# Performance work log

Hardware: AMD Instinct MI355X
Metric: run time of the kernel (lower is better)

## Reference

```python
import jax, jax.numpy as jnp
import numpy as np

C = 256
CK = C // 8  # qk projection dim


def setup_inputs() -> dict:
    key = jax.random.key(0)
    ks = jax.random.split(key, 8)
    B, H, W = 4, 64, 64
    x = jax.random.normal(ks[0], (B, C, W, H), dtype=jnp.float32)
    s = 1.0 / np.sqrt(C)
    Wf = jax.random.normal(ks[1], (CK, C), dtype=jnp.float32) * s
    bf = jax.random.normal(ks[2], (CK,), dtype=jnp.float32) * 0.01
    Wg = jax.random.normal(ks[3], (CK, C), dtype=jnp.float32) * s
    bg = jax.random.normal(ks[4], (CK,), dtype=jnp.float32) * 0.01
    Wh = jax.random.normal(ks[5], (C, C), dtype=jnp.float32) * s
    bh = jax.random.normal(ks[6], (C,), dtype=jnp.float32) * 0.01
    gamma = jax.random.normal(ks[7], (1,), dtype=jnp.float32) * 0.1
    return {"x": x, "Wf": Wf, "bf": bf, "Wg": Wg, "bg": bg,
            "Wh": Wh, "bh": bh, "gamma": gamma}


def reference(x, Wf, bf, Wg, bg, Wh, bh, gamma):
    B, Cc, Wd, Hd = x.shape
    N = Wd * Hd
    xf = x.reshape(B, Cc, N)  # B C N
    # 1x1 conv1d == channel matmul
    f = jnp.einsum('oc,bcn->bon', Wf, xf) + bf[None, :, None]  # B CK N
    g = jnp.einsum('oc,bcn->bon', Wg, xf) + bg[None, :, None]  # B CK N
    h = jnp.einsum('oc,bcn->bon', Wh, xf) + bh[None, :, None]  # B C N
    # s[b,i,j] = sum_k f[b,k,i] g[b,k,j]
    s = jnp.einsum('bki,bkj->bij', f, g)  # B N N
    attention = jax.nn.softmax(s, axis=-1)
    # out[b,c,i] = sum_j h[b,c,j] attention[b,i,j]
    out = jnp.einsum('bcj,bij->bci', h, attention)  # B C N
    out = out.reshape(B, Cc, Wd, Hd)
    return gamma[0] * out + x
```

## Files before the change

kernel.cpp:

```cpp
#include <hip/hip_runtime.h>

typedef __bf16 bf16x8 __attribute__((ext_vector_type(8)));
typedef __bf16 bf16x4 __attribute__((ext_vector_type(4)));
typedef float f32x4 __attribute__((ext_vector_type(4)));
typedef float f32x16 __attribute__((ext_vector_type(16)));

__device__ __forceinline__ f32x4 mfma16(bf16x8 a, bf16x8 b, f32x4 c) {
  return __builtin_amdgcn_mfma_f32_16x16x32_bf16(a, b, c, 0, 0, 0);
}
__device__ __forceinline__ f32x16 mfma32(bf16x8 a, bf16x8 b, f32x16 c) {
  return __builtin_amdgcn_mfma_f32_32x32x16_bf16(a, b, c, 0, 0, 0);
}

__global__ void wcvt_kernel(const float* __restrict__ Wf, const float* __restrict__ Wg,
                            const float* __restrict__ Wh, __bf16* __restrict__ Wb) {
  int i = blockIdx.x * 256 + threadIdx.x;
  float v;
  if (i < 8192)       v = Wf[i];
  else if (i < 16384) v = Wg[i - 8192];
  else                v = Wh[i - 16384];
  Wb[i] = (__bf16)v;
}

__global__ __launch_bounds__(512) void proj_kernel(
    const float* __restrict__ x, const float* __restrict__ bfv,
    const float* __restrict__ bgv, const float* __restrict__ bhv,
    const __bf16* __restrict__ Wb, __bf16* __restrict__ qkpk,
    __bf16* __restrict__ vpk) {
  __shared__ __align__(16) char smem[2560 + 18432];
  __bf16* xT = (__bf16*)smem;
  __bf16* ho = (__bf16*)(smem + 2560);

  const int t = threadIdx.x;
  const int l = t & 63, wg = t >> 6, q = l >> 4, l15 = l & 15;
  const int nh = wg & 1, oh = wg >> 1;
  const int bi = blockIdx.x;
  const int b = bi >> 7;
  const int nt = bi & 127;
  const int n0 = nt << 5;

  const float* xb = x + (size_t)b * 256 * 4096;

  f32x4 acc[5];
#pragma unroll
  for (int i = 0; i < 5; i++) acc[i] = (f32x4){0.f, 0.f, 0.f, 0.f};

  const int c_rel = t >> 4;
  const int n2 = (t & 15) * 2;

#pragma unroll 1
  for (int kc = 0; kc < 8; kc++) {
    __syncthreads();
    float2 v = *(const float2*)(xb + (size_t)(kc * 32 + c_rel) * 4096 + n0 + n2);
    xT[(n2 + 0) * 40 + c_rel] = (__bf16)v.x;
    xT[(n2 + 1) * 40 + c_rel] = (__bf16)v.y;
    __syncthreads();
    bf16x8 af = *(const bf16x8*)(xT + (nh * 16 + l15) * 40 + q * 8);
    const __bf16* wp = Wb + (size_t)(oh * 80 + l15) * 256 + kc * 32 + q * 8;
#pragma unroll
    for (int ot = 0; ot < 5; ot++) {
      bf16x8 bfr = *(const bf16x8*)(wp + (size_t)ot * 16 * 256);
      acc[ot] = mfma16(af, bfr, acc[ot]);
    }
  }

#pragma unroll
  for (int ot = 0; ot < 5; ot++) {
    int o = oh * 80 + ot * 16 + l15;
    float bias = (o < 32) ? bfv[o] : (o < 64) ? bgv[o - 32] : bhv[o - 64];
    if (oh == 0 && ot < 4) {
      int qk = o >> 5, fr = (o >> 4) & 1, hh = (o >> 3) & 1, e = o & 7;
      size_t base = ((size_t)b * 128 + nt) * 2048 + qk * 1024 + fr * 512 + hh * 256;
#pragma unroll
      for (int r = 0; r < 4; r++) {
        int n_rel = nh * 16 + q * 4 + r;
        qkpk[base + n_rel * 8 + e] = (__bf16)(acc[ot][r] + bias);
      }
    } else {
#pragma unroll
      for (int r = 0; r < 4; r++) {
        int n_rel = nh * 16 + q * 4 + r;
        ho[(o - 64) * 36 + n_rel] = (__bf16)(acc[ot][r] + bias);
      }
    }
  }
  __syncthreads();
  unsigned short* vpku = (unsigned short*)vpk + (size_t)b * 1048576;
  const unsigned short* hou = (const unsigned short*)ho;
  for (int e = t; e < 4096; e += 512) {
    int c = e >> 4, nn = (e & 15) * 2;
    int n = n0 + nn;
    int jc = n >> 4, hh = (n >> 3) & 1, ee = n & 7;
    unsigned int vv = *(const unsigned int*)(hou + c * 36 + nn);
    *(unsigned int*)(vpku + (((size_t)(jc * 2 + hh) * 256 + c) * 8 + ee)) = vv;
  }
}

__global__ __launch_bounds__(256, 3) void attn_kernel(
    const __bf16* __restrict__ qkpk, const __bf16* __restrict__ vpk,
    __bf16* __restrict__ pO, float* __restrict__ Lp) {
  __shared__ __align__(16) char smem[35072];
  __bf16* pb0 = (__bf16*)smem;
  __bf16* pb1 = (__bf16*)(smem + 17408);
  __bf16* stage = (__bf16*)smem;
  float* Lbuf = (float*)(smem + 34816);

  const int t = threadIdx.x;
  const int l = t & 63, w = t >> 6;
  const int h = l >> 5, l31 = l & 31;

  const int bi = blockIdx.x;
  const int xcd = bi & 7, slot = bi >> 3;
  const int combo = xcd * 2 + (slot & 1);
  const int b = combo >> 2, jp = combo & 3;
  const int n0 = (slot >> 1) << 6;

  const __bf16* qkb = qkpk + (size_t)b * 262144;
  const __bf16* vpb = vpk + (size_t)b * 1048576;
  const int jq0 = jp << 10;

  if (t < 64) Lbuf[t] = 0.f;

  const int it_s = w >> 1, jt = w & 1;

  const __bf16* qp = qkb + ((n0 >> 5) + it_s) * 2048 + h * 256 + l31 * 8;
  const bf16x8 qf0 = *(const bf16x8*)(qp);
  const bf16x8 qf1 = *(const bf16x8*)(qp + 512);

  f32x16 acc[2][2] = {};
  float rs[16];
#pragma unroll
  for (int r = 0; r < 16; r++) rs[r] = 0.f;

  const int vco = h * 2048 + (w * 64 + l31) * 8;

  {
    const __bf16* kp = qkb + ((jq0 >> 5) + jt) * 2048 + 1024 + h * 256 + l31 * 8;
    bf16x8 kf0 = *(const bf16x8*)(kp);
    bf16x8 kf1 = *(const bf16x8*)(kp + 512);
    f32x16 s = {};
    s = mfma32(qf0, kf0, s);
    s = mfma32(qf1, kf1, s);
#pragma unroll
    for (int r = 0; r < 16; r++) {
      float p = __expf(s[r]);
      rs[r] += p;
      int i_loc = it_s * 32 + (r & 3) + 8 * (r >> 2) + 4 * h;
      pb0[i_loc * 136 + jt * 32 + l31] = (__bf16)p;
    }
  }
  bf16x8 vf[2][4];
#pragma unroll
  for (int ci = 0; ci < 2; ci++)
#pragma unroll
    for (int kc = 0; kc < 4; kc++)
      vf[ci][kc] = *(const bf16x8*)(vpb + (size_t)((jq0 >> 4) + kc) * 4096 + vco + ci * 256);
  __syncthreads();

#pragma unroll 1
  for (int it = 0; it < 16; ++it) {
    __bf16* buf = (it & 1) ? pb1 : pb0;
    __bf16* nb  = (it & 1) ? pb0 : pb1;
    const int jn4 = (jq0 >> 4) + (((it + 1) & 15) << 2);

    bf16x8 kf0, kf1;
    if (it < 15) {
      const __bf16* kp = qkb + ((jn4 >> 1) + jt) * 2048 + 1024 + h * 256 + l31 * 8;
      kf0 = *(const bf16x8*)(kp);
      kf1 = *(const bf16x8*)(kp + 512);
    }

#pragma unroll
    for (int kc = 0; kc < 4; kc++) {
      bf16x8 pf0 = *(const bf16x8*)(buf + (size_t)(l31) * 136 + kc * 16 + h * 8);
      bf16x8 pf1 = *(const bf16x8*)(buf + (size_t)(32 + l31) * 136 + kc * 16 + h * 8);
      acc[0][0] = mfma32(pf0, vf[0][kc], acc[0][0]);
      acc[0][1] = mfma32(pf1, vf[0][kc], acc[0][1]);
      acc[1][0] = mfma32(pf0, vf[1][kc], acc[1][0]);
      acc[1][1] = mfma32(pf1, vf[1][kc], acc[1][1]);
      vf[0][kc] = *(const bf16x8*)(vpb + (size_t)(jn4 + kc) * 4096 + vco);
      vf[1][kc] = *(const bf16x8*)(vpb + (size_t)(jn4 + kc) * 4096 + vco + 256);
    }

    if (it < 15) {
      f32x16 s = {};
      s = mfma32(qf0, kf0, s);
      s = mfma32(qf1, kf1, s);
#pragma unroll
      for (int r = 0; r < 16; r++) {
        float p = __expf(s[r]);
        rs[r] += p;
        int i_loc = it_s * 32 + (r & 3) + 8 * (r >> 2) + 4 * h;
        nb[i_loc * 136 + jt * 32 + l31] = (__bf16)p;
      }
    }
    __syncthreads();
  }

#pragma unroll
  for (int r = 0; r < 16; r++) {
    float s = rs[r];
    s += __shfl_xor(s, 1, 32); s += __shfl_xor(s, 2, 32);
    s += __shfl_xor(s, 4, 32); s += __shfl_xor(s, 8, 32);
    s += __shfl_xor(s, 16, 32);
    if (l31 == 0) {
      int row = it_s * 32 + (r & 3) + 8 * (r >> 2) + 4 * h;
      atomicAdd(&Lbuf[row], s);
    }
  }

#pragma unroll
  for (int ci = 0; ci < 2; ci++) {
    int c_loc = w * 64 + ci * 32 + l31;
#pragma unroll
    for (int ii = 0; ii < 2; ii++)
#pragma unroll
      for (int r = 0; r < 16; r++) {
        int i_loc = ii * 32 + (r & 3) + 8 * (r >> 2) + 4 * h;
        stage[(size_t)c_loc * 66 + i_loc] = (__bf16)acc[ci][ii][r];
      }
  }
  __syncthreads();

  unsigned short* ob = (unsigned short*)pO + (size_t)(jp * 4 + b) * 256 * 4096 + n0;
  const unsigned short* su = (const unsigned short*)stage;
#pragma unroll 1
  for (int e = t; e < 8192; e += 256) {
    int c = e >> 5, i2 = (e & 31) * 2;
    unsigned int v = *(const unsigned int*)(su + c * 66 + i2);
    *(unsigned int*)(ob + (size_t)c * 4096 + i2) = v;
  }
  if (t < 64) Lp[(size_t)(jp * 4 + b) * 4096 + n0 + t] = Lbuf[t];
}

__global__ __launch_bounds__(256) void norm_kernel(
    const float* __restrict__ x, const float* __restrict__ gamma_p,
    const __bf16* __restrict__ pO, const float* __restrict__ Lp,
    float* __restrict__ out) {
  const int bc = blockIdx.x;
  const int b = bc >> 8;
  const float gm = gamma_p[0];
  const float* xr = x + (size_t)bc * 4096;
  float* orow = out + (size_t)bc * 4096;
  const __bf16* pbase = pO + (size_t)bc * 4096;
  const float* lbase = Lp + (size_t)b * 4096;

  for (int i0 = threadIdx.x * 4; i0 < 4096; i0 += 1024) {
    float4 xv = *(const float4*)(xr + i0);
    float s0 = 0.f, s1 = 0.f, s2 = 0.f, s3 = 0.f;
    float l0 = 0.f, l1 = 0.f, l2 = 0.f, l3 = 0.f;
#pragma unroll
    for (int jp = 0; jp < 4; jp++) {
      bf16x4 pv = *(const bf16x4*)(pbase + (size_t)jp * 4194304 + i0);
      s0 += (float)pv[0]; s1 += (float)pv[1]; s2 += (float)pv[2]; s3 += (float)pv[3];
      float4 lv = *(const float4*)(lbase + (size_t)jp * 16384 + i0);
      l0 += lv.x; l1 += lv.y; l2 += lv.z; l3 += lv.w;
    }
    float4 ov;
    ov.x = gm * s0 / l0 + xv.x;
    ov.y = gm * s1 / l1 + xv.y;
    ov.z = gm * s2 / l2 + xv.z;
    ov.w = gm * s3 / l3 + xv.w;
    *(float4*)(orow + i0) = ov;
  }
}

extern "C" void kernel_launch(void* const* d_in, const int* in_sizes, int n_in,
                              void* d_out, int out_size, void* d_ws, size_t ws_size,
                              hipStream_t stream) {
  const float* x   = (const float*)d_in[0];
  const float* Wf  = (const float*)d_in[1];
  const float* bfv = (const float*)d_in[2];
  const float* Wg  = (const float*)d_in[3];
  const float* bgv = (const float*)d_in[4];
  const float* Wh  = (const float*)d_in[5];
  const float* bhv = (const float*)d_in[6];
  const float* gm  = (const float*)d_in[7];
  float* out = (float*)d_out;

  char* ws = (char*)d_ws;
  __bf16* Wb   = (__bf16*)ws;
  __bf16* qkpk = (__bf16*)(ws + 262144);
  __bf16* vpk  = (__bf16*)(ws + 2359296);
  __bf16* pO   = (__bf16*)(ws + 10747904);
  float*  Lp   = (float*)(ws + 44302336);

  hipLaunchKernelGGL(wcvt_kernel, dim3(320), dim3(256), 0, stream, Wf, Wg, Wh, Wb);
  hipLaunchKernelGGL(proj_kernel, dim3(512), dim3(512), 0, stream,
                     x, bfv, bgv, bhv, Wb, qkpk, vpk);
  hipLaunchKernelGGL(attn_kernel, dim3(1024), dim3(256), 0, stream,
                     qkpk, vpk, pO, Lp);
  hipLaunchKernelGGL(norm_kernel, dim3(1024), dim3(256), 0, stream,
                     x, gm, pO, Lp, out);
}
```

Measured before the change: 162.3 us.

## Double attention block to 512 threads, splitting channels across eight waves

The attention kernel now runs with 512 threads (8 waves) instead of 256. The first four waves still compute the QK scores and exponentials into shared memory. All eight waves do the PV accumulation, each over 32 channels instead of 64, which halves the per-wave accumulators and V fragments. The aim is more waves for latency hiding and lower register pressure, at the cost of idle producer-side waves and larger barrier groups.

New measurement: 161.9 us. About the same (-0.3%).

```diff
diff --git a/kernel.cpp b/kernel.cpp
--- a/kernel.cpp
+++ b/kernel.cpp
@@ -96,7 +96,7 @@
   }
 }
 
-__global__ __launch_bounds__(256, 3) void attn_kernel(
+__global__ __launch_bounds__(512, 4) void attn_kernel(
     const __bf16* __restrict__ qkpk, const __bf16* __restrict__ vpk,
     __bf16* __restrict__ pO, float* __restrict__ Lp) {
   __shared__ __align__(16) char smem[35072];
@@ -108,6 +108,7 @@
   const int t = threadIdx.x;
   const int l = t & 63, w = t >> 6;
   const int h = l >> 5, l31 = l & 31;
+  const bool prod = (w < 4);
 
   const int bi = blockIdx.x;
   const int xcd = bi & 7, slot = bi >> 3;
@@ -121,20 +122,23 @@
 
   if (t < 64) Lbuf[t] = 0.f;
 
-  const int it_s = w >> 1, jt = w & 1;
-
-  const __bf16* qp = qkb + ((n0 >> 5) + it_s) * 2048 + h * 256 + l31 * 8;
-  const bf16x8 qf0 = *(const bf16x8*)(qp);
-  const bf16x8 qf1 = *(const bf16x8*)(qp + 512);
-
-  f32x16 acc[2][2] = {};
+  const int it_s = (w >> 1) & 1, jt = w & 1;
+
+  bf16x8 qf0, qf1;
+  if (prod) {
+    const __bf16* qp = qkb + ((n0 >> 5) + it_s) * 2048 + h * 256 + l31 * 8;
+    qf0 = *(const bf16x8*)(qp);
+    qf1 = *(const bf16x8*)(qp + 512);
+  }
+
+  f32x16 acc[2] = {};
   float rs[16];
 #pragma unroll
   for (int r = 0; r < 16; r++) rs[r] = 0.f;
 
-  const int vco = h * 2048 + (w * 64 + l31) * 8;
-
-  {
+  const int vco = h * 2048 + (w * 32 + l31) * 8;
+
+  if (prod) {
     const __bf16* kp = qkb + ((jq0 >> 5) + jt) * 2048 + 1024 + h * 256 + l31 * 8;
     bf16x8 kf0 = *(const bf16x8*)(kp);
     bf16x8 kf1 = *(const bf16x8*)(kp + 512);
@@ -149,12 +153,10 @@
       pb0[i_loc * 136 + jt * 32 + l31] = (__bf16)p;
     }
   }
-  bf16x8 vf[2][4];
-#pragma unroll
-  for (int ci = 0; ci < 2; ci++)
-#pragma unroll
-    for (int kc = 0; kc < 4; kc++)
-      vf[ci][kc] = *(const bf16x8*)(vpb + (size_t)((jq0 >> 4) + kc) * 4096 + vco + ci * 256);
+  bf16x8 vf[4];
+#pragma unroll
+  for (int kc = 0; kc < 4; kc++)
+    vf[kc] = *(const bf16x8*)(vpb + (size_t)((jq0 >> 4) + kc) * 4096 + vco);
   __syncthreads();
 
 #pragma unroll 1
@@ -164,7 +166,7 @@
     const int jn4 = (jq0 >> 4) + (((it + 1) & 15) << 2);
 
     bf16x8 kf0, kf1;
-    if (it < 15) {
+    if (prod && it < 15) {
       const __bf16* kp = qkb + ((jn4 >> 1) + jt) * 2048 + 1024 + h * 256 + l31 * 8;
       kf0 = *(const bf16x8*)(kp);
       kf1 = *(const bf16x8*)(kp + 512);
@@ -174,15 +176,12 @@
     for (int kc = 0; kc < 4; kc++) {
       bf16x8 pf0 = *(const bf16x8*)(buf + (size_t)(l31) * 136 + kc * 16 + h * 8);
       bf16x8 pf1 = *(const bf16x8*)(buf + (size_t)(32 + l31) * 136 + kc * 16 + h * 8);
-      acc[0][0] = mfma32(pf0, vf[0][kc], acc[0][0]);
-      acc[0][1] = mfma32(pf1, vf[0][kc], acc[0][1]);
-      acc[1][0] = mfma32(pf0, vf[1][kc], acc[1][0]);
-      acc[1][1] = mfma32(pf1, vf[1][kc], acc[1][1]);
-      vf[0][kc] = *(const bf16x8*)(vpb + (size_t)(jn4 + kc) * 4096 + vco);
-      vf[1][kc] = *(const bf16x8*)(vpb + (size_t)(jn4 + kc) * 4096 + vco + 256);
-    }
-
-    if (it < 15) {
+      acc[0] = mfma32(pf0, vf[kc], acc[0]);
+      acc[1] = mfma32(pf1, vf[kc], acc[1]);
+      vf[kc] = *(const bf16x8*)(vpb + (size_t)(jn4 + kc) * 4096 + vco);
+    }
+
+    if (prod && it < 15) {
       f32x16 s = {};
       s = mfma32(qf0, kf0, s);
       s = mfma32(qf1, kf1, s);
@@ -197,27 +196,28 @@
     __syncthreads();
   }
 
-#pragma unroll
-  for (int r = 0; r < 16; r++) {
-    float s = rs[r];
-    s += __shfl_xor(s, 1, 32); s += __shfl_xor(s, 2, 32);
-    s += __shfl_xor(s, 4, 32); s += __shfl_xor(s, 8, 32);
-    s += __shfl_xor(s, 16, 32);
-    if (l31 == 0) {
-      int row = it_s * 32 + (r & 3) + 8 * (r >> 2) + 4 * h;
-      atomicAdd(&Lbuf[row], s);
-    }
-  }
-
-#pragma unroll
-  for (int ci = 0; ci < 2; ci++) {
-    int c_loc = w * 64 + ci * 32 + l31;
+  if (prod) {
+#pragma unroll
+    for (int r = 0; r < 16; r++) {
+      float s = rs[r];
+      s += __shfl_xor(s, 1, 32); s += __shfl_xor(s, 2, 32);
+      s += __shfl_xor(s, 4, 32); s += __shfl_xor(s, 8, 32);
+      s += __shfl_xor(s, 16, 32);
+      if (l31 == 0) {
+        int row = it_s * 32 + (r & 3) + 8 * (r >> 2) + 4 * h;
+        atomicAdd(&Lbuf[row], s);
+      }
+    }
+  }
+
+  {
+    int c_loc = w * 32 + l31;
 #pragma unroll
     for (int ii = 0; ii < 2; ii++)
 #pragma unroll
       for (int r = 0; r < 16; r++) {
         int i_loc = ii * 32 + (r & 3) + 8 * (r >> 2) + 4 * h;
-        stage[(size_t)c_loc * 66 + i_loc] = (__bf16)acc[ci][ii][r];
+        stage[(size_t)c_loc * 66 + i_loc] = (__bf16)acc[ii][r];
       }
   }
   __syncthreads();
@@ -225,7 +225,7 @@
   unsigned short* ob = (unsigned short*)pO + (size_t)(jp * 4 + b) * 256 * 4096 + n0;
   const unsigned short* su = (const unsigned short*)stage;
 #pragma unroll 1
-  for (int e = t; e < 8192; e += 256) {
+  for (int e = t; e < 8192; e += 512) {
     int c = e >> 5, i2 = (e & 31) * 2;
     unsigned int v = *(const unsigned int*)(su + c * 66 + i2);
     *(unsigned int*)(ob + (size_t)c * 4096 + i2) = v;
@@ -288,7 +288,7 @@
   hipLaunchKernelGGL(wcvt_kernel, dim3(320), dim3(256), 0, stream, Wf, Wg, Wh, Wb);
   hipLaunchKernelGGL(proj_kernel, dim3(512), dim3(512), 0, stream,
                      x, bfv, bgv, bhv, Wb, qkpk, vpk);
-  hipLaunchKernelGGL(attn_kernel, dim3(1024), dim3(256), 0, stream,
+  hipLaunchKernelGGL(attn_kernel, dim3(1024), dim3(512), 0, stream,
                      qkpk, vpk, pO, Lp);
   hipLaunchKernelGGL(norm_kernel, dim3(1024), dim3(256), 0, stream,
                      x, gm, pO, Lp, out);
```

## Keep attention probabilities in registers via permlane swap, one query tile per wave

Applied to the files above, without the earlier changes.

Restructures the attention kernel so each wave owns a 32-row query tile across all 256 channels. It computes S transposed (K as A operand) and repacks exp(S) into MFMA A-operand layout with v_permlane32_swap. This removes the LDS round trip and the block-wide barriers on P that the old kernel needed each iteration. The cost is 8 accumulators per wave and V fragments loaded per wave rather than shared across waves, so global/L2 V traffic rises and blocks become 512 threads with a large LDS staging area.

New measurement: 162.0 us. No clear change (-0.2%).

```diff
diff --git a/kernel.cpp b/kernel.cpp
--- a/kernel.cpp
+++ b/kernel.cpp
@@ -10,6 +10,15 @@
 }
 __device__ __forceinline__ f32x16 mfma32(bf16x8 a, bf16x8 b, f32x16 c) {
   return __builtin_amdgcn_mfma_f32_32x32x16_bf16(a, b, c, 0, 0, 0);
+}
+
+__device__ __forceinline__ unsigned int cvtpk(float a, float b) {
+  union { __bf16 h[2]; unsigned int u; } r;
+  r.h[0] = (__bf16)a; r.h[1] = (__bf16)b;
+  return r.u;
+}
+__device__ __forceinline__ void swap32(unsigned int &a, unsigned int &b) {
+  asm("v_permlane32_swap_b32 %0, %1" : "+v"(a), "+v"(b));
 }
 
 __global__ void wcvt_kernel(const float* __restrict__ Wf, const float* __restrict__ Wg,
@@ -96,141 +105,106 @@
   }
 }
 
-__global__ __launch_bounds__(256, 3) void attn_kernel(
+__global__ __launch_bounds__(512, 2) void attn_kernel(
     const __bf16* __restrict__ qkpk, const __bf16* __restrict__ vpk,
     __bf16* __restrict__ pO, float* __restrict__ Lp) {
-  __shared__ __align__(16) char smem[35072];
-  __bf16* pb0 = (__bf16*)smem;
-  __bf16* pb1 = (__bf16*)(smem + 17408);
-  __bf16* stage = (__bf16*)smem;
-  float* Lbuf = (float*)(smem + 34816);
+  __shared__ __align__(16) char smem[139264];
 
   const int t = threadIdx.x;
   const int l = t & 63, w = t >> 6;
   const int h = l >> 5, l31 = l & 31;
 
   const int bi = blockIdx.x;
-  const int xcd = bi & 7, slot = bi >> 3;
-  const int combo = xcd * 2 + (slot & 1);
+  const int xcd = bi & 7;
+  const int combo = xcd * 2 + ((bi >> 3) & 1);
+  const int ig = bi >> 4;
   const int b = combo >> 2, jp = combo & 3;
-  const int n0 = (slot >> 1) << 6;
+  const int ti = ig * 8 + w;
+  const int n0 = ti << 5;
 
   const __bf16* qkb = qkpk + (size_t)b * 262144;
   const __bf16* vpb = vpk + (size_t)b * 1048576;
   const int jq0 = jp << 10;
 
-  if (t < 64) Lbuf[t] = 0.f;
-
-  const int it_s = w >> 1, jt = w & 1;
-
-  const __bf16* qp = qkb + ((n0 >> 5) + it_s) * 2048 + h * 256 + l31 * 8;
+  const __bf16* qp = qkb + (size_t)ti * 2048 + h * 256 + l31 * 8;
   const bf16x8 qf0 = *(const bf16x8*)(qp);
   const bf16x8 qf1 = *(const bf16x8*)(qp + 512);
 
-  f32x16 acc[2][2] = {};
-  float rs[16];
-#pragma unroll
-  for (int r = 0; r < 16; r++) rs[r] = 0.f;
-
-  const int vco = h * 2048 + (w * 64 + l31) * 8;
-
-  {
-    const __bf16* kp = qkb + ((jq0 >> 5) + jt) * 2048 + 1024 + h * 256 + l31 * 8;
-    bf16x8 kf0 = *(const bf16x8*)(kp);
-    bf16x8 kf1 = *(const bf16x8*)(kp + 512);
+  f32x16 acc[8] = {};
+  float rsum = 0.f;
+
+  const __bf16* kbase = qkb + 1024 + h * 256 + l31 * 8;
+  const int vlane = h * 2048 + l31 * 8;
+
+  bf16x8 kf0 = *(const bf16x8*)(kbase + (size_t)(jq0 >> 5) * 2048);
+  bf16x8 kf1 = *(const bf16x8*)(kbase + (size_t)(jq0 >> 5) * 2048 + 512);
+
+#pragma unroll 1
+  for (int ch = 0; ch < 32; ++ch) {
     f32x16 s = {};
-    s = mfma32(qf0, kf0, s);
-    s = mfma32(qf1, kf1, s);
-#pragma unroll
-    for (int r = 0; r < 16; r++) {
-      float p = __expf(s[r]);
-      rs[r] += p;
-      int i_loc = it_s * 32 + (r & 3) + 8 * (r >> 2) + 4 * h;
-      pb0[i_loc * 136 + jt * 32 + l31] = (__bf16)p;
-    }
-  }
-  bf16x8 vf[2][4];
-#pragma unroll
-  for (int ci = 0; ci < 2; ci++)
-#pragma unroll
-    for (int kc = 0; kc < 4; kc++)
-      vf[ci][kc] = *(const bf16x8*)(vpb + (size_t)((jq0 >> 4) + kc) * 4096 + vco + ci * 256);
-  __syncthreads();
-
-#pragma unroll 1
-  for (int it = 0; it < 16; ++it) {
-    __bf16* buf = (it & 1) ? pb1 : pb0;
-    __bf16* nb  = (it & 1) ? pb0 : pb1;
-    const int jn4 = (jq0 >> 4) + (((it + 1) & 15) << 2);
-
-    bf16x8 kf0, kf1;
-    if (it < 15) {
-      const __bf16* kp = qkb + ((jn4 >> 1) + jt) * 2048 + 1024 + h * 256 + l31 * 8;
+    s = mfma32(kf0, qf0, s);
+    s = mfma32(kf1, qf1, s);
+
+    if (ch < 31) {
+      const __bf16* kp = kbase + (size_t)((jq0 >> 5) + ch + 1) * 2048;
       kf0 = *(const bf16x8*)(kp);
       kf1 = *(const bf16x8*)(kp + 512);
     }
 
-#pragma unroll
-    for (int kc = 0; kc < 4; kc++) {
-      bf16x8 pf0 = *(const bf16x8*)(buf + (size_t)(l31) * 136 + kc * 16 + h * 8);
-      bf16x8 pf1 = *(const bf16x8*)(buf + (size_t)(32 + l31) * 136 + kc * 16 + h * 8);
-      acc[0][0] = mfma32(pf0, vf[0][kc], acc[0][0]);
-      acc[0][1] = mfma32(pf1, vf[0][kc], acc[0][1]);
-      acc[1][0] = mfma32(pf0, vf[1][kc], acc[1][0]);
-      acc[1][1] = mfma32(pf1, vf[1][kc], acc[1][1]);
-      vf[0][kc] = *(const bf16x8*)(vpb + (size_t)(jn4 + kc) * 4096 + vco);
-      vf[1][kc] = *(const bf16x8*)(vpb + (size_t)(jn4 + kc) * 4096 + vco + 256);
-    }
-
-    if (it < 15) {
-      f32x16 s = {};
-      s = mfma32(qf0, kf0, s);
-      s = mfma32(qf1, kf1, s);
-#pragma unroll
-      for (int r = 0; r < 16; r++) {
-        float p = __expf(s[r]);
-        rs[r] += p;
-        int i_loc = it_s * 32 + (r & 3) + 8 * (r >> 2) + 4 * h;
-        nb[i_loc * 136 + jt * 32 + l31] = (__bf16)p;
-      }
-    }
-    __syncthreads();
-  }
-
-#pragma unroll
-  for (int r = 0; r < 16; r++) {
-    float s = rs[r];
-    s += __shfl_xor(s, 1, 32); s += __shfl_xor(s, 2, 32);
-    s += __shfl_xor(s, 4, 32); s += __shfl_xor(s, 8, 32);
-    s += __shfl_xor(s, 16, 32);
-    if (l31 == 0) {
-      int row = it_s * 32 + (r & 3) + 8 * (r >> 2) + 4 * h;
-      atomicAdd(&Lbuf[row], s);
-    }
-  }
-
-#pragma unroll
-  for (int ci = 0; ci < 2; ci++) {
-    int c_loc = w * 64 + ci * 32 + l31;
-#pragma unroll
-    for (int ii = 0; ii < 2; ii++)
-#pragma unroll
-      for (int r = 0; r < 16; r++) {
-        int i_loc = ii * 32 + (r & 3) + 8 * (r >> 2) + 4 * h;
-        stage[(size_t)c_loc * 66 + i_loc] = (__bf16)acc[ci][ii][r];
-      }
-  }
-  __syncthreads();
-
-  unsigned short* ob = (unsigned short*)pO + (size_t)(jp * 4 + b) * 256 * 4096 + n0;
+    const __bf16* vchunk = vpb + (size_t)((jq0 >> 4) + ch * 2) * 4096 + vlane;
+    bf16x8 vb0[8];
+#pragma unroll
+    for (int ct = 0; ct < 8; ct++)
+      vb0[ct] = *(const bf16x8*)(vchunk + ct * 256);
+
+    float p[16];
+#pragma unroll
+    for (int r = 0; r < 16; r++) { p[r] = __expf(s[r]); rsum += p[r]; }
+
+    unsigned int u0 = cvtpk(p[0], p[1]), v0 = cvtpk(p[2], p[3]);
+    unsigned int w0 = cvtpk(p[4], p[5]), z0 = cvtpk(p[6], p[7]);
+    swap32(u0, w0); swap32(v0, z0);
+    unsigned int u1 = cvtpk(p[8], p[9]), v1 = cvtpk(p[10], p[11]);
+    unsigned int w1 = cvtpk(p[12], p[13]), z1 = cvtpk(p[14], p[15]);
+    swap32(u1, w1); swap32(v1, z1);
+    union { unsigned int u[4]; bf16x8 v; } A0, A1;
+    A0.u[0] = u0; A0.u[1] = v0; A0.u[2] = w0; A0.u[3] = z0;
+    A1.u[0] = u1; A1.u[1] = v1; A1.u[2] = w1; A1.u[3] = z1;
+
+    bf16x8 vb1[8];
+#pragma unroll
+    for (int ct = 0; ct < 8; ct++)
+      vb1[ct] = *(const bf16x8*)(vchunk + 4096 + ct * 256);
+
+#pragma unroll
+    for (int ct = 0; ct < 8; ct++) acc[ct] = mfma32(A0.v, vb0[ct], acc[ct]);
+#pragma unroll
+    for (int ct = 0; ct < 8; ct++) acc[ct] = mfma32(A1.v, vb1[ct], acc[ct]);
+  }
+
+  __bf16* stage = (__bf16*)smem + (size_t)w * 8704;
+#pragma unroll
+  for (int ct = 0; ct < 8; ct++) {
+    int c0 = ct * 32 + l31;
+#pragma unroll
+    for (int r = 0; r < 16; r++) {
+      int i_loc = (r & 3) + 8 * (r >> 2) + 4 * h;
+      stage[c0 * 34 + i_loc] = (__bf16)acc[ct][r];
+    }
+  }
+  asm volatile("s_waitcnt lgkmcnt(0)" ::: "memory");
+
+  unsigned short* ob = (unsigned short*)pO + (size_t)(jp * 4 + b) * 1048576 + n0;
   const unsigned short* su = (const unsigned short*)stage;
 #pragma unroll 1
-  for (int e = t; e < 8192; e += 256) {
-    int c = e >> 5, i2 = (e & 31) * 2;
-    unsigned int v = *(const unsigned int*)(su + c * 66 + i2);
-    *(unsigned int*)(ob + (size_t)c * 4096 + i2) = v;
-  }
-  if (t < 64) Lp[(size_t)(jp * 4 + b) * 4096 + n0 + t] = Lbuf[t];
+  for (int e = l; e < 4096; e += 64) {
+    int c = e >> 4, i2 = (e & 15) * 2;
+    unsigned int vv = *(const unsigned int*)(su + c * 34 + i2);
+    *(unsigned int*)(ob + (size_t)c * 4096 + i2) = vv;
+  }
+
+  rsum += __shfl_xor(rsum, 32);
+  if (l < 32) Lp[(size_t)(jp * 4 + b) * 4096 + n0 + l] = rsum;
 }
 
 __global__ __launch_bounds__(256) void norm_kernel(
@@ -288,7 +262,7 @@
   hipLaunchKernelGGL(wcvt_kernel, dim3(320), dim3(256), 0, stream, Wf, Wg, Wh, Wb);
   hipLaunchKernelGGL(proj_kernel, dim3(512), dim3(512), 0, stream,
                      x, bfv, bgv, bhv, Wb, qkpk, vpk);
-  hipLaunchKernelGGL(attn_kernel, dim3(1024), dim3(256), 0, stream,
+  hipLaunchKernelGGL(attn_kernel, dim3(256), dim3(512), 0, stream,
                      qkpk, vpk, pO, Lp);
   hipLaunchKernelGGL(norm_kernel, dim3(1024), dim3(256), 0, stream,
                      x, gm, pO, Lp, out);
```
